# Optimization experiments

Measured on AMD Instinct MI355X. Metric: run time of the kernel, lower is better.

The kernel has to match this reference:

```python
import jax, jax.numpy as jnp
import numpy as np

NUM_GRAPHS = 1000


def _gine_conv(x, src, dst, edge_attr, w_e, b_e, w1, b1, w2, b2):
    # GINEConv (eps=0): out = nn(x + sum_{j->i} relu(x_j + lin_edge(e_ji)))
    e = edge_attr @ w_e + b_e                      # [E, F]
    m = jax.nn.relu(x[src] + e)                    # [E, F] per-edge message
    agg = jnp.zeros_like(x).at[dst].add(m)         # [N, F] scatter-add to targets
    h = x + agg
    h = jax.nn.relu(h @ w1 + b1)
    h = jax.nn.relu(h @ w2 + b2)
    return h


def _segment_softmax(scores, seg, num_segments):
    m = jax.ops.segment_max(scores, seg, num_segments=num_segments)
    z = jnp.exp(scores - m[seg])
    s = jax.ops.segment_sum(z, seg, num_segments=num_segments)
    return z / s[seg]


def setup_inputs() -> dict:
    key = jax.random.key(0)
    ks = jax.random.split(key, 16)
    N, E, F_IN, H, ED = 100000, 1600000, 9, 64, 1

    x = jax.random.normal(ks[0], (N, F_IN), dtype=jnp.float32)
    edge_index = jax.random.randint(ks[1], (2, E), 0, N, dtype=jnp.int32)
    edge_attr = jax.random.normal(ks[2], (E, ED), dtype=jnp.float32)
    batch = jnp.sort(jax.random.randint(ks[3], (N,), 0, NUM_GRAPHS, dtype=jnp.int32))
    B_total = jax.random.uniform(ks[4], (NUM_GRAPHS,), dtype=jnp.float32)

    def lin(k, fi, fo):
        k1, k2 = jax.random.split(k)
        bound = 1.0 / np.sqrt(fi)
        w = jax.random.uniform(k1, (fi, fo), minval=-bound, maxval=bound, dtype=jnp.float32)
        b = jax.random.uniform(k2, (fo,), minval=-bound, maxval=bound, dtype=jnp.float32)
        return w, b

    we1, be1 = lin(ks[5], ED, F_IN)    # conv1 edge projection -> in_channels
    w11, b11 = lin(ks[6], F_IN, H)
    w12, b12 = lin(ks[7], H, H)
    we2, be2 = lin(ks[8], ED, H)       # conv2 edge projection
    w21, b21 = lin(ks[9], H, H)
    w22, b22 = lin(ks[10], H, H)
    wr1, br1 = lin(ks[11], H, H // 2)
    wr2, br2 = lin(ks[12], H // 2, 1)

    return {"x": x, "edge_index": edge_index, "edge_attr": edge_attr,
            "batch": batch, "B_total": B_total,
            "we1": we1, "be1": be1, "w11": w11, "b11": b11, "w12": w12, "b12": b12,
            "we2": we2, "be2": be2, "w21": w21, "b21": b21, "w22": w22, "b22": b22,
            "wr1": wr1, "br1": br1, "wr2": wr2, "br2": br2}


def reference(x, edge_index, edge_attr, batch, B_total,
              we1, be1, w11, b11, w12, b12,
              we2, be2, w21, b21, w22, b22,
              wr1, br1, wr2, br2):
    src, dst = edge_index[0], edge_index[1]
    h = _gine_conv(x, src, dst, edge_attr, we1, be1, w11, b11, w12, b12)
    h = _gine_conv(h, src, dst, edge_attr, we2, be2, w21, b21, w22, b22)
    raw = (jax.nn.relu(h @ wr1 + br1) @ wr2 + br2)[:, 0]   # [N]
    alloc_probs = _segment_softmax(raw, batch, NUM_GRAPHS)
    return alloc_probs * B_total[batch]
```

## Files before the change

kernel.cpp:

```cpp
#include <hip/hip_runtime.h>
#include <float.h>

__global__ void deg_rank_kernel(const int* __restrict__ dst, int* __restrict__ deg,
                                int* __restrict__ rank, int E) {
  int j = blockIdx.x * blockDim.x + threadIdx.x;
  if (j < E) rank[j] = atomicAdd(&deg[dst[j]], 1);
}

__global__ void scan_pass1(const int* __restrict__ deg, int* __restrict__ blocksum, int N) {
  __shared__ int sdata[1024];
  int i = blockIdx.x * 1024 + threadIdx.x;
  sdata[threadIdx.x] = (i < N) ? deg[i] : 0;
  __syncthreads();
  for (int s = 512; s > 0; s >>= 1) {
    if (threadIdx.x < s) sdata[threadIdx.x] += sdata[threadIdx.x + s];
    __syncthreads();
  }
  if (threadIdx.x == 0) blocksum[blockIdx.x] = sdata[0];
}

__global__ void scan_pass2(int* __restrict__ blocksum, int nb) {
  __shared__ int sdata[1024];
  int t = threadIdx.x;
  sdata[t] = (t < nb) ? blocksum[t] : 0;
  __syncthreads();
  if (t == 0) {
    int run = 0;
    for (int i = 0; i < nb; ++i) { int v = sdata[i]; sdata[i] = run; run += v; }
  }
  __syncthreads();
  if (t < nb) blocksum[t] = sdata[t];
}

__global__ void scan_pass3(const int* __restrict__ deg, const int* __restrict__ blocksum,
                           int* __restrict__ rowptr, int N, int E) {
  __shared__ int sdata[1024];
  int i = blockIdx.x * 1024 + threadIdx.x;
  int v = (i < N) ? deg[i] : 0;
  sdata[threadIdx.x] = v;
  __syncthreads();
  for (int off = 1; off < 1024; off <<= 1) {
    int t = (threadIdx.x >= off) ? sdata[threadIdx.x - off] : 0;
    __syncthreads();
    sdata[threadIdx.x] += t;
    __syncthreads();
  }
  if (i < N) rowptr[i] = blocksum[blockIdx.x] + sdata[threadIdx.x] - v;
  if (i == 0) rowptr[N] = E;
}

__global__ void scatter_kernel(const int* __restrict__ dst, const int* __restrict__ rank,
                               const int* __restrict__ rowptr,
                               const int* __restrict__ src, const float* __restrict__ ea,
                               int2* __restrict__ epack, int E) {
  int j = blockIdx.x * blockDim.x + threadIdx.x;
  if (j >= E) return;
  int pos = rowptr[dst[j]] + rank[j];
  epack[pos] = make_int2(src[j], __float_as_int(ea[j]));
}

__global__ void __launch_bounds__(256, 8) gather1_kernel(
    const float* __restrict__ x, const int* __restrict__ rowptr,
    const int2* __restrict__ epack,
    const float* __restrict__ we1, const float* __restrict__ be1,
    float* __restrict__ xin, int N) {
  int i = blockIdx.x * blockDim.x + threadIdx.x;
  if (i >= N) return;
  float we[9], be[9];
#pragma unroll
  for (int f = 0; f < 9; ++f) { we[f] = we1[f]; be[f] = be1[f]; }
  float acc[9];
#pragma unroll
  for (int f = 0; f < 9; ++f) acc[f] = 0.0f;

  int p0 = rowptr[i], p1 = rowptr[i + 1];
  int p = p0;
  for (; p + 1 < p1; p += 2) {
    int2 e0 = epack[p], e1 = epack[p + 1];
    float a0 = __int_as_float(e0.y), a1 = __int_as_float(e1.y);
    float r0[9], r1[9];
#pragma unroll
    for (int f = 0; f < 9; ++f) r0[f] = x[(size_t)e0.x * 9 + f];
#pragma unroll
    for (int f = 0; f < 9; ++f) r1[f] = x[(size_t)e1.x * 9 + f];
#pragma unroll
    for (int f = 0; f < 9; ++f) {
      acc[f] += fmaxf(fmaf(a0, we[f], be[f]) + r0[f], 0.0f);
      acc[f] += fmaxf(fmaf(a1, we[f], be[f]) + r1[f], 0.0f);
    }
  }
  for (; p < p1; ++p) {
    int2 e = epack[p];
    float a = __int_as_float(e.y);
#pragma unroll
    for (int f = 0; f < 9; ++f)
      acc[f] += fmaxf(fmaf(a, we[f], be[f]) + x[(size_t)e.x * 9 + f], 0.0f);
  }
#pragma unroll
  for (int f = 0; f < 9; ++f) xin[(size_t)i * 9 + f] = x[(size_t)i * 9 + f] + acc[f];
}

__global__ void __launch_bounds__(256, 3) node1_mlp(
    const float* __restrict__ xin,
    const float* __restrict__ w11, const float* __restrict__ b11,
    const float* __restrict__ w12, const float* __restrict__ b12,
    unsigned short* __restrict__ h1b, int N) {
  __shared__ float sW1[9 * 64];
  __shared__ float sB1[64];
  __shared__ float sW2t[64 * 64];
  __shared__ float sB2[64];
  __shared__ unsigned short tile[256][66];
  for (int t = threadIdx.x; t < 9 * 64; t += blockDim.x) sW1[t] = w11[t];
  for (int t = threadIdx.x; t < 64 * 64; t += blockDim.x) {
    int o = t >> 6, k = t & 63;
    sW2t[t] = w12[k * 64 + o];
  }
  for (int t = threadIdx.x; t < 64; t += blockDim.x) { sB1[t] = b11[t]; sB2[t] = b12[t]; }
  __syncthreads();
  int i0 = blockIdx.x * 256;
  int i = i0 + threadIdx.x;
  if (i < N) {
    float xv[9];
#pragma unroll
    for (int k = 0; k < 9; ++k) xv[k] = xin[(size_t)i * 9 + k];
    float t1[64];
#pragma unroll
    for (int o = 0; o < 64; ++o) {
      float a = sB1[o];
#pragma unroll
      for (int k = 0; k < 9; ++k) a = fmaf(xv[k], sW1[k * 64 + o], a);
      t1[o] = fmaxf(a, 0.0f);
    }
#pragma unroll
    for (int o = 0; o < 64; ++o) {
      float a = sB2[o];
#pragma unroll
      for (int k = 0; k < 64; k += 4) {
        float4 wv = *(const float4*)(sW2t + o * 64 + k);
        a = fmaf(t1[k], wv.x, a);
        a = fmaf(t1[k + 1], wv.y, a);
        a = fmaf(t1[k + 2], wv.z, a);
        a = fmaf(t1[k + 3], wv.w, a);
      }
      float v = fmaxf(a, 0.0f);
      unsigned u = __float_as_uint(v);
      tile[threadIdx.x][o] = (unsigned short)((u + 0x7FFFu + ((u >> 16) & 1u)) >> 16);
    }
  }
  __syncthreads();
#pragma unroll
  for (int it = 0; it < 16; ++it) {
    int idx = it * 256 + threadIdx.x;
    int r = idx >> 4;
    int c = idx & 15;
    if (i0 + r < N) {
      const unsigned short* tp = &tile[r][c * 4];
      uint2 v;
      v.x = (unsigned)tp[0] | ((unsigned)tp[1] << 16);
      v.y = (unsigned)tp[2] | ((unsigned)tp[3] << 16);
      *(uint2*)(h1b + (size_t)(i0 + r) * 64 + c * 4) = v;
    }
  }
}

__device__ __forceinline__ float4 bf4_to_f4(uint2 u) {
  float4 r;
  r.x = __uint_as_float(u.x << 16);
  r.y = __uint_as_float(u.x & 0xFFFF0000u);
  r.z = __uint_as_float(u.y << 16);
  r.w = __uint_as_float(u.y & 0xFFFF0000u);
  return r;
}

__global__ void __launch_bounds__(256, 8) gather2_kernel(
    const unsigned short* __restrict__ h1b, const int* __restrict__ rowptr,
    const int2* __restrict__ epack,
    const float* __restrict__ we2, const float* __restrict__ be2,
    float* __restrict__ agg2, int N) {
  int wid = threadIdx.x >> 6;
  int lane = threadIdx.x & 63;
  int g = lane >> 4;
  int l = lane & 15;
  int i = blockIdx.x * 4 + wid;
  if (i >= N) return;

  float4 we_l = *(const float4*)(we2 + 4 * l);
  float4 be_l = *(const float4*)(be2 + 4 * l);
  float4 acc = make_float4(0.f, 0.f, 0.f, 0.f);

  int p0 = rowptr[i], p1 = rowptr[i + 1];
  int p = p0 + g;
  for (; p + 4 < p1; p += 8) {
    int2 e0 = epack[p], e1 = epack[p + 4];
    float a0 = __int_as_float(e0.y), a1 = __int_as_float(e1.y);
    float4 h0 = bf4_to_f4(*(const uint2*)(h1b + (size_t)e0.x * 64 + 4 * l));
    float4 hv = bf4_to_f4(*(const uint2*)(h1b + (size_t)e1.x * 64 + 4 * l));
    acc.x += fmaxf(fmaf(a0, we_l.x, be_l.x) + h0.x, 0.f);
    acc.y += fmaxf(fmaf(a0, we_l.y, be_l.y) + h0.y, 0.f);
    acc.z += fmaxf(fmaf(a0, we_l.z, be_l.z) + h0.z, 0.f);
    acc.w += fmaxf(fmaf(a0, we_l.w, be_l.w) + h0.w, 0.f);
    acc.x += fmaxf(fmaf(a1, we_l.x, be_l.x) + hv.x, 0.f);
    acc.y += fmaxf(fmaf(a1, we_l.y, be_l.y) + hv.y, 0.f);
    acc.z += fmaxf(fmaf(a1, we_l.z, be_l.z) + hv.z, 0.f);
    acc.w += fmaxf(fmaf(a1, we_l.w, be_l.w) + hv.w, 0.f);
  }
  for (; p < p1; p += 4) {
    int2 e = epack[p];
    float a = __int_as_float(e.y);
    float4 h = bf4_to_f4(*(const uint2*)(h1b + (size_t)e.x * 64 + 4 * l));
    acc.x += fmaxf(fmaf(a, we_l.x, be_l.x) + h.x, 0.f);
    acc.y += fmaxf(fmaf(a, we_l.y, be_l.y) + h.y, 0.f);
    acc.z += fmaxf(fmaf(a, we_l.z, be_l.z) + h.z, 0.f);
    acc.w += fmaxf(fmaf(a, we_l.w, be_l.w) + h.w, 0.f);
  }
#pragma unroll
  for (int off = 16; off <= 32; off <<= 1) {
    acc.x += __shfl_xor(acc.x, off);
    acc.y += __shfl_xor(acc.y, off);
    acc.z += __shfl_xor(acc.z, off);
    acc.w += __shfl_xor(acc.w, off);
  }
  if (g == 0) {
    float4 hs = bf4_to_f4(*(const uint2*)(h1b + (size_t)i * 64 + 4 * l));
    acc.x += hs.x; acc.y += hs.y; acc.z += hs.z; acc.w += hs.w;
    *(float4*)(agg2 + (size_t)i * 64 + 4 * l) = acc;
  }
}

__global__ void __launch_bounds__(256, 2) node2_kernel(
    const float* __restrict__ agg2,
    const float* __restrict__ w21, const float* __restrict__ b21,
    const float* __restrict__ w22, const float* __restrict__ b22,
    const float* __restrict__ wr1, const float* __restrict__ br1,
    const float* __restrict__ wr2, const float* __restrict__ br2,
    float* __restrict__ raw, int N, int chunk) {
  __shared__ float sW1t[64 * 64];
  __shared__ float sW2t[64 * 64];
  __shared__ float sWr1t[32 * 64];
  __shared__ float sB1[64];
  __shared__ float sB2[64];
  __shared__ float sBr1[32];
  __shared__ float sWr2[32];
  __shared__ float sBr2;
  for (int t = threadIdx.x; t < 64 * 64; t += blockDim.x) {
    int o = t >> 6, k = t & 63;
    sW1t[t] = w21[k * 64 + o];
    sW2t[t] = w22[k * 64 + o];
  }
  for (int t = threadIdx.x; t < 32 * 64; t += blockDim.x) {
    int o = t >> 6, k = t & 63;
    sWr1t[t] = wr1[k * 32 + o];
  }
  for (int t = threadIdx.x; t < 64; t += blockDim.x) { sB1[t] = b21[t]; sB2[t] = b22[t]; }
  for (int t = threadIdx.x; t < 32; t += blockDim.x) { sBr1[t] = br1[t]; sWr2[t] = wr2[t]; }
  if (threadIdx.x == 0) sBr2 = br2[0];
  __syncthreads();
  int i = blockIdx.x * chunk + threadIdx.x;
  if ((int)threadIdx.x >= chunk || i >= N) return;
  float hin[64];
#pragma unroll
  for (int k = 0; k < 64; k += 4) {
    float4 v = *(const float4*)(agg2 + (size_t)i * 64 + k);
    hin[k] = v.x; hin[k + 1] = v.y; hin[k + 2] = v.z; hin[k + 3] = v.w;
  }
  float a1[64];
#pragma unroll
  for (int o = 0; o < 64; ++o) {
    float acc = sB1[o];
#pragma unroll
    for (int k = 0; k < 64; k += 4) {
      float4 wv = *(const float4*)(sW1t + o * 64 + k);
      acc = fmaf(hin[k], wv.x, acc);
      acc = fmaf(hin[k + 1], wv.y, acc);
      acc = fmaf(hin[k + 2], wv.z, acc);
      acc = fmaf(hin[k + 3], wv.w, acc);
    }
    a1[o] = fmaxf(acc, 0.0f);
  }
  float a2[64];
#pragma unroll
  for (int o = 0; o < 64; ++o) {
    float acc = sB2[o];
#pragma unroll
    for (int k = 0; k < 64; k += 4) {
      float4 wv = *(const float4*)(sW2t + o * 64 + k);
      acc = fmaf(a1[k], wv.x, acc);
      acc = fmaf(a1[k + 1], wv.y, acc);
      acc = fmaf(a1[k + 2], wv.z, acc);
      acc = fmaf(a1[k + 3], wv.w, acc);
    }
    a2[o] = fmaxf(acc, 0.0f);
  }
  float r[32];
#pragma unroll
  for (int o = 0; o < 32; ++o) {
    float acc = sBr1[o];
#pragma unroll
    for (int k = 0; k < 64; k += 4) {
      float4 wv = *(const float4*)(sWr1t + o * 64 + k);
      acc = fmaf(a2[k], wv.x, acc);
      acc = fmaf(a2[k + 1], wv.y, acc);
      acc = fmaf(a2[k + 2], wv.z, acc);
      acc = fmaf(a2[k + 3], wv.w, acc);
    }
    r[o] = fmaxf(acc, 0.0f);
  }
  float acc = sBr2;
#pragma unroll
  for (int k = 0; k < 32; ++k) acc = fmaf(r[k], sWr2[k], acc);
  raw[i] = acc;
}

__device__ __forceinline__ int lowerb(const int* __restrict__ a, int n, int key) {
  int lo = 0, hi = n;
  while (lo < hi) { int mid = (lo + hi) >> 1; if (a[mid] < key) lo = mid + 1; else hi = mid; }
  return lo;
}

__global__ void segsoftmax_kernel(const float* __restrict__ raw, const int* __restrict__ batch,
                                  const float* __restrict__ Btot, float* __restrict__ out, int N) {
  __shared__ float sred[256];
  int g = blockIdx.x;
  int tid = threadIdx.x;
  int start = lowerb(batch, N, g);
  int end = lowerb(batch, N, g + 1);
  if (start >= end) return;

  float m = -FLT_MAX;
  for (int i = start + tid; i < end; i += 256) m = fmaxf(m, raw[i]);
  sred[tid] = m;
  __syncthreads();
  for (int s = 128; s > 0; s >>= 1) {
    if (tid < s) sred[tid] = fmaxf(sred[tid], sred[tid + s]);
    __syncthreads();
  }
  m = sred[0];
  __syncthreads();

  float sum = 0.0f;
  for (int i = start + tid; i < end; i += 256) sum += expf(raw[i] - m);
  sred[tid] = sum;
  __syncthreads();
  for (int s = 128; s > 0; s >>= 1) {
    if (tid < s) sred[tid] += sred[tid + s];
    __syncthreads();
  }
  float scale = Btot[g] / sred[0];

  for (int i = start + tid; i < end; i += 256) out[i] = expf(raw[i] - m) * scale;
}

extern "C" void kernel_launch(void* const* d_in, const int* in_sizes, int n_in,
                              void* d_out, int out_size, void* d_ws, size_t ws_size,
                              hipStream_t stream) {
  const float* x     = (const float*)d_in[0];
  const int* eidx    = (const int*)d_in[1];
  const float* eattr = (const float*)d_in[2];
  const int* batch   = (const int*)d_in[3];
  const float* Btot  = (const float*)d_in[4];
  const float* we1 = (const float*)d_in[5];
  const float* be1 = (const float*)d_in[6];
  const float* w11 = (const float*)d_in[7];
  const float* b11 = (const float*)d_in[8];
  const float* w12 = (const float*)d_in[9];
  const float* b12 = (const float*)d_in[10];
  const float* we2 = (const float*)d_in[11];
  const float* be2 = (const float*)d_in[12];
  const float* w21 = (const float*)d_in[13];
  const float* b21 = (const float*)d_in[14];
  const float* w22 = (const float*)d_in[15];
  const float* b22 = (const float*)d_in[16];
  const float* wr1 = (const float*)d_in[17];
  const float* br1 = (const float*)d_in[18];
  const float* wr2 = (const float*)d_in[19];
  const float* br2 = (const float*)d_in[20];

  const int N  = in_sizes[0] / 9;
  const int E  = in_sizes[2];
  const int NG = in_sizes[4];
  const int* src = eidx;
  const int* dst = eidx + E;

  const int NB = (N + 1023) / 1024;

  char* w = (char*)d_ws;
  int*   deg    = (int*)w;                 w += (size_t)N * 4;
  int*   rowptr = (int*)w;                 w += (size_t)(N + 1) * 4;
  int*   blocksum = (int*)w;               w += (size_t)1024 * 4;
  int*   rank   = (int*)w;                 w += (size_t)E * 4;
  int2*  epack  = (int2*)w;                w += (size_t)E * 8;
  unsigned short* h1b = (unsigned short*)w; w += (size_t)N * 64 * 2;
  float* agg2   = (float*)w;               w += (size_t)N * 64 * 4;
  float* raw    = (float*)w;               w += (size_t)N * 4;
  float* xin = agg2;

  hipMemsetAsync(deg, 0, (size_t)N * 4, stream);

  dim3 blk(256);
  dim3 egrid((E + 255) / 256);
  dim3 ngrid((N + 255) / 256);

  deg_rank_kernel<<<egrid, blk, 0, stream>>>(dst, deg, rank, E);
  scan_pass1<<<dim3(NB), dim3(1024), 0, stream>>>(deg, blocksum, N);
  scan_pass2<<<dim3(1), dim3(1024), 0, stream>>>(blocksum, NB);
  scan_pass3<<<dim3(NB), dim3(1024), 0, stream>>>(deg, blocksum, rowptr, N, E);
  scatter_kernel<<<egrid, blk, 0, stream>>>(dst, rank, rowptr, src, eattr, epack, E);

  gather1_kernel<<<ngrid, blk, 0, stream>>>(x, rowptr, epack, we1, be1, xin, N);
  node1_mlp<<<ngrid, blk, 0, stream>>>(xin, w11, b11, w12, b12, h1b, N);

  dim3 l2grid((N + 3) / 4);
  gather2_kernel<<<l2grid, blk, 0, stream>>>(h1b, rowptr, epack, we2, be2, agg2, N);
  const int N2B = 512;
  const int chunk = (N + N2B - 1) / N2B;
  node2_kernel<<<dim3(N2B), blk, 0, stream>>>(agg2, w21, b21, w22, b22,
                                              wr1, br1, wr2, br2, raw, N, chunk);

  segsoftmax_kernel<<<dim3(NG), blk, 0, stream>>>(raw, batch, Btot, (float*)d_out, N);
}
```

Baseline: 300.0 us.

## Replace random CSR scatter with two-pass bucketed binning by destination range

The single random scatter of edges into CSR order becomes two passes. First, edges are binned into 64 coarse buckets keyed on destination>>11, using per-block shared-memory counts and global cursors. Then each bucket's packed records are scattered to their final CSR slots, so writes land in a localized address window for better cache and write locality. In exchange it adds an extra E*16-byte intermediate buffer, an extra edge pass with shared atomics, and bucket counting inside the degree kernel, which now uses a fixed grid-stride launch.

```diff
diff --git a/kernel.cpp b/kernel.cpp
--- a/kernel.cpp
+++ b/kernel.cpp
@@ -1,10 +1,27 @@
 #include <hip/hip_runtime.h>
 #include <float.h>
 
+#define NBK 64
+#define EPB 8192
+
+__device__ __forceinline__ unsigned short bf16rne(float f) {
+  unsigned u = __float_as_uint(f);
+  return (unsigned short)((u + 0x7FFFu + ((u >> 16) & 1u)) >> 16);
+}
+
 __global__ void deg_rank_kernel(const int* __restrict__ dst, int* __restrict__ deg,
-                                int* __restrict__ rank, int E) {
-  int j = blockIdx.x * blockDim.x + threadIdx.x;
-  if (j < E) rank[j] = atomicAdd(&deg[dst[j]], 1);
+                                int* __restrict__ rank, int* __restrict__ bkcount, int E) {
+  __shared__ int lcnt[NBK];
+  if (threadIdx.x < NBK) lcnt[threadIdx.x] = 0;
+  __syncthreads();
+  for (int j = blockIdx.x * blockDim.x + threadIdx.x; j < E; j += gridDim.x * blockDim.x) {
+    int d = dst[j];
+    rank[j] = atomicAdd(&deg[d], 1);
+    atomicAdd(&lcnt[d >> 11], 1);
+  }
+  __syncthreads();
+  if (threadIdx.x < NBK && lcnt[threadIdx.x] > 0)
+    atomicAdd(&bkcount[threadIdx.x], lcnt[threadIdx.x]);
 }
 
 __global__ void scan_pass1(const int* __restrict__ deg, int* __restrict__ blocksum, int N) {
@@ -19,7 +36,8 @@
   if (threadIdx.x == 0) blocksum[blockIdx.x] = sdata[0];
 }
 
-__global__ void scan_pass2(int* __restrict__ blocksum, int nb) {
+__global__ void scan_pass2(int* __restrict__ blocksum, int nb,
+                           const int* __restrict__ bkcount, int* __restrict__ bkcursor) {
   __shared__ int sdata[1024];
   int t = threadIdx.x;
   sdata[t] = (t < nb) ? blocksum[t] : 0;
@@ -27,6 +45,8 @@
   if (t == 0) {
     int run = 0;
     for (int i = 0; i < nb; ++i) { int v = sdata[i]; sdata[i] = run; run += v; }
+    int brun = 0;
+    for (int i = 0; i < NBK; ++i) { int v = bkcount[i]; bkcursor[i] = brun; brun += v; }
   }
   __syncthreads();
   if (t < nb) blocksum[t] = sdata[t];
@@ -49,14 +69,38 @@
   if (i == 0) rowptr[N] = E;
 }
 
-__global__ void scatter_kernel(const int* __restrict__ dst, const int* __restrict__ rank,
-                               const int* __restrict__ rowptr,
-                               const int* __restrict__ src, const float* __restrict__ ea,
-                               int2* __restrict__ epack, int E) {
+__global__ void binA_kernel(const int* __restrict__ dst, const int* __restrict__ src,
+                            const float* __restrict__ ea, const int* __restrict__ rank,
+                            int* __restrict__ bkcursor, int4* __restrict__ epk4, int E) {
+  __shared__ int lcnt[NBK];
+  __shared__ int lbase[NBK];
+  int e0 = blockIdx.x * EPB;
+  int e1 = min(e0 + EPB, E);
+  if (threadIdx.x < NBK) lcnt[threadIdx.x] = 0;
+  __syncthreads();
+  for (int j = e0 + threadIdx.x; j < e1; j += 256)
+    atomicAdd(&lcnt[dst[j] >> 11], 1);
+  __syncthreads();
+  if (threadIdx.x < NBK) {
+    int c = lcnt[threadIdx.x];
+    lbase[threadIdx.x] = (c > 0) ? atomicAdd(&bkcursor[threadIdx.x], c) : 0;
+    lcnt[threadIdx.x] = 0;
+  }
+  __syncthreads();
+  for (int j = e0 + threadIdx.x; j < e1; j += 256) {
+    int d = dst[j];
+    int bk = d >> 11;
+    int ofs = atomicAdd(&lcnt[bk], 1);
+    epk4[lbase[bk] + ofs] = make_int4(src[j], __float_as_int(ea[j]), d, rank[j]);
+  }
+}
+
+__global__ void binB_kernel(const int4* __restrict__ epk4, const int* __restrict__ rowptr,
+                            int2* __restrict__ epack, int E) {
   int j = blockIdx.x * blockDim.x + threadIdx.x;
   if (j >= E) return;
-  int pos = rowptr[dst[j]] + rank[j];
-  epack[pos] = make_int2(src[j], __float_as_int(ea[j]));
+  int4 v = epk4[j];
+  epack[rowptr[v.z] + v.w] = make_int2(v.x, v.y);
 }
 
 __global__ void __launch_bounds__(256, 8) gather1_kernel(
@@ -142,9 +186,7 @@
         a = fmaf(t1[k + 2], wv.z, a);
         a = fmaf(t1[k + 3], wv.w, a);
       }
-      float v = fmaxf(a, 0.0f);
-      unsigned u = __float_as_uint(v);
-      tile[threadIdx.x][o] = (unsigned short)((u + 0x7FFFu + ((u >> 16) & 1u)) >> 16);
+      tile[threadIdx.x][o] = bf16rne(fmaxf(a, 0.0f));
     }
   }
   __syncthreads();
@@ -385,26 +427,31 @@
 
   char* w = (char*)d_ws;
   int*   deg    = (int*)w;                 w += (size_t)N * 4;
+  int*   bkcount = (int*)w;                w += (size_t)NBK * 4;
+  int*   bkcursor = (int*)w;               w += (size_t)NBK * 4;
   int*   rowptr = (int*)w;                 w += (size_t)(N + 1) * 4;
   int*   blocksum = (int*)w;               w += (size_t)1024 * 4;
   int*   rank   = (int*)w;                 w += (size_t)E * 4;
+  int4*  epk4   = (int4*)w;                w += (size_t)E * 16;
   int2*  epack  = (int2*)w;                w += (size_t)E * 8;
   unsigned short* h1b = (unsigned short*)w; w += (size_t)N * 64 * 2;
   float* agg2   = (float*)w;               w += (size_t)N * 64 * 4;
   float* raw    = (float*)w;               w += (size_t)N * 4;
   float* xin = agg2;
 
-  hipMemsetAsync(deg, 0, (size_t)N * 4, stream);
+  hipMemsetAsync(deg, 0, ((size_t)N + NBK) * 4, stream);
 
   dim3 blk(256);
   dim3 egrid((E + 255) / 256);
   dim3 ngrid((N + 255) / 256);
 
-  deg_rank_kernel<<<egrid, blk, 0, stream>>>(dst, deg, rank, E);
+  deg_rank_kernel<<<dim3(512), blk, 0, stream>>>(dst, deg, rank, bkcount, E);
   scan_pass1<<<dim3(NB), dim3(1024), 0, stream>>>(deg, blocksum, N);
-  scan_pass2<<<dim3(1), dim3(1024), 0, stream>>>(blocksum, NB);
+  scan_pass2<<<dim3(1), dim3(1024), 0, stream>>>(blocksum, NB, bkcount, bkcursor);
   scan_pass3<<<dim3(NB), dim3(1024), 0, stream>>>(deg, blocksum, rowptr, N, E);
-  scatter_kernel<<<egrid, blk, 0, stream>>>(dst, rank, rowptr, src, eattr, epack, E);
+  binA_kernel<<<dim3((E + EPB - 1) / EPB), blk, 0, stream>>>(dst, src, eattr, rank,
+                                                             bkcursor, epk4, E);
+  binB_kernel<<<egrid, blk, 0, stream>>>(epk4, rowptr, epack, E);
 
   gather1_kernel<<<ngrid, blk, 0, stream>>>(x, rowptr, epack, we1, be1, xin, N);
   node1_mlp<<<ngrid, blk, 0, stream>>>(xin, w11, b11, w12, b12, h1b, N);
```

New measurement: 330.8 us. +10.3%, slower.

## Replace global-atomic CSR build with two-level bucketed binning sort

Applied to the files above, without the earlier changes.

Replaces the per-edge global atomic degree/rank counting, three-pass scan and random scatter with a two-level bucket sort. Edges are first binned by dst>>10 into 98 coarse buckets using shared-memory histograms, then each bucket builds its rowptr and edge list with LDS atomics. This is meant to cut contention on global atomics and make the scatter writes more local, at the cost of an extra 16-byte-per-edge intermediate pass. The layout within each node's edge list is now nondeterministic and assumes nbk ≤ 128.

```diff
diff --git a/kernel.cpp b/kernel.cpp
--- a/kernel.cpp
+++ b/kernel.cpp
@@ -1,62 +1,104 @@
 #include <hip/hip_runtime.h>
 #include <float.h>
 
-__global__ void deg_rank_kernel(const int* __restrict__ dst, int* __restrict__ deg,
-                                int* __restrict__ rank, int E) {
-  int j = blockIdx.x * blockDim.x + threadIdx.x;
-  if (j < E) rank[j] = atomicAdd(&deg[dst[j]], 1);
-}
-
-__global__ void scan_pass1(const int* __restrict__ deg, int* __restrict__ blocksum, int N) {
-  __shared__ int sdata[1024];
-  int i = blockIdx.x * 1024 + threadIdx.x;
-  sdata[threadIdx.x] = (i < N) ? deg[i] : 0;
-  __syncthreads();
-  for (int s = 512; s > 0; s >>= 1) {
-    if (threadIdx.x < s) sdata[threadIdx.x] += sdata[threadIdx.x + s];
+#define NBKCAP 128
+#define EPB 8192
+
+__device__ __forceinline__ unsigned short bf16rne(float f) {
+  unsigned u = __float_as_uint(f);
+  return (unsigned short)((u + 0x7FFFu + ((u >> 16) & 1u)) >> 16);
+}
+
+__global__ void bkhist_kernel(const int* __restrict__ dst, int* __restrict__ bkcount,
+                              int E, int nbk) {
+  __shared__ int lcnt[NBKCAP];
+  for (int t = threadIdx.x; t < nbk; t += 256) lcnt[t] = 0;
+  __syncthreads();
+  for (int j = blockIdx.x * 256 + threadIdx.x; j < E; j += gridDim.x * 256)
+    atomicAdd(&lcnt[dst[j] >> 10], 1);
+  __syncthreads();
+  for (int t = threadIdx.x; t < nbk; t += 256)
+    if (lcnt[t]) atomicAdd(&bkcount[t], lcnt[t]);
+}
+
+__global__ void bkscan_kernel(const int* __restrict__ bkcount, int* __restrict__ bkbase,
+                              int* __restrict__ bkcursor, int nbk, int E) {
+  if (threadIdx.x == 0) {
+    int run = 0;
+    for (int i = 0; i < nbk; ++i) { bkbase[i] = run; bkcursor[i] = run; run += bkcount[i]; }
+    bkbase[nbk] = E;
+  }
+}
+
+__global__ void binA_kernel(const int* __restrict__ dst, const int* __restrict__ src,
+                            const float* __restrict__ ea,
+                            int* __restrict__ bkcursor, int4* __restrict__ epk4,
+                            int E, int nbk) {
+  __shared__ int lcnt[NBKCAP];
+  __shared__ int lbase[NBKCAP];
+  int e0 = blockIdx.x * EPB;
+  int e1 = min(e0 + EPB, E);
+  for (int t = threadIdx.x; t < nbk; t += 256) lcnt[t] = 0;
+  __syncthreads();
+  for (int j = e0 + threadIdx.x; j < e1; j += 256)
+    atomicAdd(&lcnt[dst[j] >> 10], 1);
+  __syncthreads();
+  for (int t = threadIdx.x; t < nbk; t += 256) {
+    int c = lcnt[t];
+    lbase[t] = c ? atomicAdd(&bkcursor[t], c) : 0;
+    lcnt[t] = 0;
+  }
+  __syncthreads();
+  for (int j = e0 + threadIdx.x; j < e1; j += 256) {
+    int d = dst[j];
+    int bk = d >> 10;
+    int ofs = atomicAdd(&lcnt[bk], 1);
+    epk4[lbase[bk] + ofs] = make_int4(src[j], __float_as_int(ea[j]), d, 0);
+  }
+}
+
+__global__ void bucket_build(const int4* __restrict__ epk4, const int* __restrict__ bkbase,
+                             int* __restrict__ rowptr, int2* __restrict__ epack,
+                             int N, int E) {
+  __shared__ int ldeg[1024];
+  __shared__ int lsum[256];
+  int bk = blockIdx.x;
+  int node0 = bk << 10;
+  int s0 = bkbase[bk], s1 = bkbase[bk + 1];
+  for (int t = threadIdx.x; t < 1024; t += 256) ldeg[t] = 0;
+  __syncthreads();
+  for (int p = s0 + threadIdx.x; p < s1; p += 256)
+    atomicAdd(&ldeg[epk4[p].z & 1023], 1);
+  __syncthreads();
+  int base = threadIdx.x * 4;
+  int v0 = ldeg[base], v1 = ldeg[base + 1], v2 = ldeg[base + 2], v3 = ldeg[base + 3];
+  int s = v0 + v1 + v2 + v3;
+  lsum[threadIdx.x] = s;
+  __syncthreads();
+  for (int off = 1; off < 256; off <<= 1) {
+    int t = (threadIdx.x >= off) ? lsum[threadIdx.x - off] : 0;
     __syncthreads();
-  }
-  if (threadIdx.x == 0) blocksum[blockIdx.x] = sdata[0];
-}
-
-__global__ void scan_pass2(int* __restrict__ blocksum, int nb) {
-  __shared__ int sdata[1024];
-  int t = threadIdx.x;
-  sdata[t] = (t < nb) ? blocksum[t] : 0;
-  __syncthreads();
-  if (t == 0) {
-    int run = 0;
-    for (int i = 0; i < nb; ++i) { int v = sdata[i]; sdata[i] = run; run += v; }
-  }
-  __syncthreads();
-  if (t < nb) blocksum[t] = sdata[t];
-}
-
-__global__ void scan_pass3(const int* __restrict__ deg, const int* __restrict__ blocksum,
-                           int* __restrict__ rowptr, int N, int E) {
-  __shared__ int sdata[1024];
-  int i = blockIdx.x * 1024 + threadIdx.x;
-  int v = (i < N) ? deg[i] : 0;
-  sdata[threadIdx.x] = v;
-  __syncthreads();
-  for (int off = 1; off < 1024; off <<= 1) {
-    int t = (threadIdx.x >= off) ? sdata[threadIdx.x - off] : 0;
+    lsum[threadIdx.x] += t;
     __syncthreads();
-    sdata[threadIdx.x] += t;
-    __syncthreads();
-  }
-  if (i < N) rowptr[i] = blocksum[blockIdx.x] + sdata[threadIdx.x] - v;
-  if (i == 0) rowptr[N] = E;
-}
-
-__global__ void scatter_kernel(const int* __restrict__ dst, const int* __restrict__ rank,
-                               const int* __restrict__ rowptr,
-                               const int* __restrict__ src, const float* __restrict__ ea,
-                               int2* __restrict__ epack, int E) {
-  int j = blockIdx.x * blockDim.x + threadIdx.x;
-  if (j >= E) return;
-  int pos = rowptr[dst[j]] + rank[j];
-  epack[pos] = make_int2(src[j], __float_as_int(ea[j]));
+  }
+  int ex = lsum[threadIdx.x] - s;
+  __syncthreads();
+  ldeg[base]     = s0 + ex;
+  ldeg[base + 1] = s0 + ex + v0;
+  ldeg[base + 2] = s0 + ex + v0 + v1;
+  ldeg[base + 3] = s0 + ex + v0 + v1 + v2;
+  __syncthreads();
+  for (int t = threadIdx.x; t < 1024; t += 256) {
+    int node = node0 + t;
+    if (node < N) rowptr[node] = ldeg[t];
+  }
+  __syncthreads();
+  for (int p = s0 + threadIdx.x; p < s1; p += 256) {
+    int4 v = epk4[p];
+    int pos = atomicAdd(&ldeg[v.z & 1023], 1);
+    epack[pos] = make_int2(v.x, v.y);
+  }
+  if (bk == 0 && threadIdx.x == 0) rowptr[N] = E;
 }
 
 __global__ void __launch_bounds__(256, 8) gather1_kernel(
@@ -142,9 +184,7 @@
         a = fmaf(t1[k + 2], wv.z, a);
         a = fmaf(t1[k + 3], wv.w, a);
       }
-      float v = fmaxf(a, 0.0f);
-      unsigned u = __float_as_uint(v);
-      tile[threadIdx.x][o] = (unsigned short)((u + 0x7FFFu + ((u >> 16) & 1u)) >> 16);
+      tile[threadIdx.x][o] = bf16rne(fmaxf(a, 0.0f));
     }
   }
   __syncthreads();
@@ -381,30 +421,30 @@
   const int* src = eidx;
   const int* dst = eidx + E;
 
-  const int NB = (N + 1023) / 1024;
+  const int nbk = (N + 1023) >> 10;
 
   char* w = (char*)d_ws;
-  int*   deg    = (int*)w;                 w += (size_t)N * 4;
+  int*   bkcount = (int*)w;                w += (size_t)NBKCAP * 4;
+  int*   bkbase  = (int*)w;                w += (size_t)(NBKCAP + 1) * 4;
+  int*   bkcursor = (int*)w;               w += (size_t)NBKCAP * 4;
   int*   rowptr = (int*)w;                 w += (size_t)(N + 1) * 4;
-  int*   blocksum = (int*)w;               w += (size_t)1024 * 4;
-  int*   rank   = (int*)w;                 w += (size_t)E * 4;
+  int4*  epk4   = (int4*)w;                w += (size_t)E * 16;
   int2*  epack  = (int2*)w;                w += (size_t)E * 8;
   unsigned short* h1b = (unsigned short*)w; w += (size_t)N * 64 * 2;
   float* agg2   = (float*)w;               w += (size_t)N * 64 * 4;
   float* raw    = (float*)w;               w += (size_t)N * 4;
   float* xin = agg2;
 
-  hipMemsetAsync(deg, 0, (size_t)N * 4, stream);
+  hipMemsetAsync(bkcount, 0, (size_t)NBKCAP * 4, stream);
 
   dim3 blk(256);
-  dim3 egrid((E + 255) / 256);
   dim3 ngrid((N + 255) / 256);
 
-  deg_rank_kernel<<<egrid, blk, 0, stream>>>(dst, deg, rank, E);
-  scan_pass1<<<dim3(NB), dim3(1024), 0, stream>>>(deg, blocksum, N);
-  scan_pass2<<<dim3(1), dim3(1024), 0, stream>>>(blocksum, NB);
-  scan_pass3<<<dim3(NB), dim3(1024), 0, stream>>>(deg, blocksum, rowptr, N, E);
-  scatter_kernel<<<egrid, blk, 0, stream>>>(dst, rank, rowptr, src, eattr, epack, E);
+  bkhist_kernel<<<dim3(1024), blk, 0, stream>>>(dst, bkcount, E, nbk);
+  bkscan_kernel<<<dim3(1), dim3(64), 0, stream>>>(bkcount, bkbase, bkcursor, nbk, E);
+  binA_kernel<<<dim3((E + EPB - 1) / EPB), blk, 0, stream>>>(dst, src, eattr,
+                                                             bkcursor, epk4, E, nbk);
+  bucket_build<<<dim3(nbk), blk, 0, stream>>>(epk4, bkbase, rowptr, epack, N, E);
 
   gather1_kernel<<<ngrid, blk, 0, stream>>>(x, rowptr, epack, we1, be1, xin, N);
   node1_mlp<<<ngrid, blk, 0, stream>>>(xin, w11, b11, w12, b12, h1b, N);
```

New measurement: 308.1 us. 2.7% more time.
